# Kernel optimization log

Hardware: AMD Instinct MI355X
Metric: run time of the kernel (lower is better)

Reference implementation:

```python
import jax, jax.numpy as jnp
import numpy as np

B, N, L = 1, 256, 512
D_MSA, D_STATE, D_INNER, D_FF = 256, 64, 32, 1024
H = 4
CA_IDX = 1
SCALE = (D_STATE // H) ** -0.5
BINS = np.array([8.0, 12.0, 16.0, 20.0], dtype=np.float32)
EPS = 1e-5


def _ln(x, g, b):
    m = x.mean(-1, keepdims=True)
    v = ((x - m) ** 2).mean(-1, keepdims=True)
    return (x - m) * jax.lax.rsqrt(v + EPS) * g + b


def setup_inputs() -> dict:
    key = jax.random.key(0)
    ks = jax.random.split(key, 8)
    w = lambda k, shp: (jax.random.normal(k, shp, dtype=jnp.float32) * 0.02)
    return {
        "xyz": jax.random.normal(ks[0], (B, L, 3, 3), dtype=jnp.float32) * 10.0,
        "state": jax.random.normal(ks[1], (B, L, D_STATE), dtype=jnp.float32),
        "msa": jax.random.normal(ks[2], (B, N, L, D_MSA), dtype=jnp.float32),
        "ln_msa_g": jnp.ones((D_MSA,)), "ln_msa_b": jnp.zeros((D_MSA,)),
        "ln_state_g": jnp.ones((D_STATE,)), "ln_state_b": jnp.zeros((D_STATE,)),
        "Wq": w(ks[3], (D_STATE, H * D_INNER)), "bq": jnp.zeros((H * D_INNER,)),
        "Wk": w(ks[4], (D_STATE, H * D_INNER)), "bk": jnp.zeros((H * D_INNER,)),
        "Wv": w(ks[5], (D_MSA, D_MSA)), "bv": jnp.zeros((D_MSA,)),
        "ln_out_g": jnp.ones((D_MSA,)), "ln_out_b": jnp.zeros((D_MSA,)),
        "ff_ln_g": jnp.ones((D_MSA,)), "ff_ln_b": jnp.zeros((D_MSA,)),
        "W1": w(ks[6], (D_MSA, D_FF)), "b1": jnp.zeros((D_FF,)),
        "W2": w(ks[7], (D_FF, D_MSA)), "b2": jnp.zeros((D_MSA,)),
    }


def reference(xyz, state, msa, ln_msa_g, ln_msa_b, ln_state_g, ln_state_b,
              Wq, bq, Wk, bk, Wv, bv, ln_out_g, ln_out_b,
              ff_ln_g, ff_ln_b, W1, b1, W2, b2):
    state_n = _ln(state, ln_state_g, ln_state_b)          # [b,l,ds]
    msa_n = _ln(msa, ln_msa_g, ln_msa_b)                  # [b,n,l,dm]

    q = (state_n @ Wq + bq).reshape(B, L, H, D_INNER).transpose(0, 2, 1, 3)  # bhld
    k = (state_n @ Wk + bk).reshape(B, L, H, D_INNER).transpose(0, 2, 1, 3)
    v = (msa_n @ Wv + bv).reshape(B, N, L, H, D_MSA // H).transpose(0, 3, 1, 2, 4)  # bhnld

    ca = xyz[:, :, CA_IDX]                                # [b,l,3]
    diff = ca[:, :, None, :] - ca[:, None, :, :]
    pdist = jnp.sqrt((diff * diff).sum(-1))               # [b,l,l]
    mask = (pdist[:, None] < jnp.asarray(BINS)[None, :, None, None]).astype(state.dtype)  # [b,h,l,l]

    logits = jnp.einsum('bhid,bhjd->bhij', q * SCALE, k) + (1.0 - mask) * -1e9
    att = jax.nn.softmax(logits, axis=-1)                 # [b,h,i,j]

    out = jnp.einsum('bhij,bhnjd->bhnid', att, v)         # [b,h,n,l,d]
    out = out.transpose(0, 2, 3, 1, 4).reshape(B, N, L, D_MSA)

    msa2 = msa_n + _ln(out, ln_out_g, ln_out_b)
    hdn = jnp.maximum(_ln(msa2, ff_ln_g, ff_ln_b) @ W1 + b1, 0.0)
    return msa2 + hdn @ W2 + b2
```

## Files before the change

kernel.cpp:

```cpp
#include <hip/hip_runtime.h>
#include <stdint.h>

typedef __attribute__((ext_vector_type(8))) short bf16x8;
typedef __attribute__((ext_vector_type(4))) float f32x4;
typedef __attribute__((ext_vector_type(4))) short s16x4;

__device__ __forceinline__ float bf2f(short u) {
  union { float f; unsigned int i; } c; c.i = ((unsigned int)(unsigned short)u) << 16; return c.f;
}
__device__ __forceinline__ short f2bf(float f) {
  union { float f; unsigned int i; } c; c.f = f;
  return (short)((c.i + 0x7FFFu + ((c.i >> 16) & 1u)) >> 16);
}
__device__ __forceinline__ float wredsum(float v) {
#pragma unroll
  for (int o = 32; o; o >>= 1) v += __shfl_xor(v, o);
  return v;
}
__device__ __forceinline__ void gload16(const short* g, short* l) {
  __builtin_amdgcn_global_load_lds(
      (const __attribute__((address_space(1))) unsigned int*)g,
      (__attribute__((address_space(3))) unsigned int*)l, 16, 0, 0);
}

__global__ void k_transpose(const float* __restrict__ in, short* __restrict__ out,
                            int R, int C) {
  int idx = blockIdx.x * 256 + threadIdx.x;
  if (idx >= R * C) return;
  int c = idx / R, r = idx - c * R;
  out[idx] = f2bf(in[(size_t)r * C + c]);
}

__global__ __launch_bounds__(128) void k_qk(
    const float* __restrict__ state, const float* __restrict__ g, const float* __restrict__ b,
    const float* __restrict__ Wq, const float* __restrict__ bq,
    const float* __restrict__ Wk, const float* __restrict__ bk,
    float* __restrict__ qbuf, float* __restrict__ kbuf) {
  __shared__ float sn[64];
  const int l = blockIdx.x, tid = threadIdx.x;
  if (tid < 64) {
    float v = state[l * 64 + tid];
    float mean = wredsum(v) * (1.f / 64.f);
    float d = v - mean;
    float var = wredsum(d * d) * (1.f / 64.f);
    sn[tid] = d * rsqrtf(var + 1e-5f) * g[tid] + b[tid];
  }
  __syncthreads();
  float qa = 0.f, ka = 0.f;
#pragma unroll 8
  for (int k = 0; k < 64; ++k) {
    float s = sn[k];
    qa += s * Wq[k * 128 + tid];
    ka += s * Wk[k * 128 + tid];
  }
  qbuf[l * 128 + tid] = (qa + bq[tid]) * 0.25f;
  kbuf[l * 128 + tid] = ka + bk[tid];
}

__global__ __launch_bounds__(256) void k_att(
    const float* __restrict__ qbuf, const float* __restrict__ kbuf,
    const float* __restrict__ xyz, short* __restrict__ att) {
  __shared__ float qs[32];
  __shared__ float cai[3];
  __shared__ float wm[4], wsm[4];
  const int i = blockIdx.x, h = blockIdx.y, t = threadIdx.x;
  if (t < 32) qs[t] = qbuf[i * 128 + h * 32 + t];
  if (t < 3) cai[t] = xyz[i * 9 + 3 + t];
  __syncthreads();
  const float bin2 = (h == 0) ? 64.f : (h == 1) ? 144.f : (h == 2) ? 256.f : 400.f;
  float lg[2];
#pragma unroll
  for (int p = 0; p < 2; ++p) {
    int j = t + p * 256;
    const float* kr = kbuf + j * 128 + h * 32;
    float a = 0.f;
#pragma unroll 8
    for (int d = 0; d < 32; ++d) a += qs[d] * kr[d];
    float dx = cai[0] - xyz[j * 9 + 3], dy = cai[1] - xyz[j * 9 + 4], dz = cai[2] - xyz[j * 9 + 5];
    float d2 = dx * dx + dy * dy + dz * dz;
    lg[p] = (d2 < bin2) ? a : a - 1e9f;
  }
  const int wave = t >> 6, lane = t & 63;
  float m = fmaxf(lg[0], lg[1]);
#pragma unroll
  for (int o = 32; o; o >>= 1) m = fmaxf(m, __shfl_xor(m, o));
  if (lane == 0) wm[wave] = m;
  __syncthreads();
  m = fmaxf(fmaxf(wm[0], wm[1]), fmaxf(wm[2], wm[3]));
  float e0 = __expf(lg[0] - m), e1 = __expf(lg[1] - m);
  float s = wredsum(e0 + e1);
  if (lane == 0) wsm[wave] = s;
  __syncthreads();
  float inv = 1.f / (wsm[0] + wsm[1] + wsm[2] + wsm[3]);
  size_t base = ((size_t)h * 512 + i) * 512;
  att[base + t] = f2bf(e0 * inv);
  att[base + t + 256] = f2bf(e1 * inv);
}

__global__ __launch_bounds__(256) void k_msaln(
    const float* __restrict__ msa, const float* __restrict__ g, const float* __restrict__ b,
    short* __restrict__ msa_n) {
  const int wave = threadIdx.x >> 6, lane = threadIdx.x & 63;
  const size_t row = (size_t)blockIdx.x * 4 + wave;
  const float4 v = ((const float4*)(msa + row * 256))[lane];
  float mean = wredsum(v.x + v.y + v.z + v.w) * (1.f / 256.f);
  float d0 = v.x - mean, d1 = v.y - mean, d2 = v.z - mean, d3 = v.w - mean;
  float var = wredsum(d0 * d0 + d1 * d1 + d2 * d2 + d3 * d3) * (1.f / 256.f);
  float rs = rsqrtf(var + 1e-5f);
  const int c = lane * 4;
  s16x4 o;
  o[0] = f2bf(d0 * rs * g[c + 0] + b[c + 0]);
  o[1] = f2bf(d1 * rs * g[c + 1] + b[c + 1]);
  o[2] = f2bf(d2 * rs * g[c + 2] + b[c + 2]);
  o[3] = f2bf(d3 * rs * g[c + 3] + b[c + 3]);
  *(s16x4*)(msa_n + row * 256 + c) = o;
}

__global__ __launch_bounds__(256) void k_msa2(
    const short* __restrict__ O, const float* __restrict__ bv,
    const short* __restrict__ msa_n,
    const float* __restrict__ go, const float* __restrict__ bo,
    const float* __restrict__ gf, const float* __restrict__ bfp,
    short* __restrict__ msa2, short* __restrict__ msa2ln) {
  const int wave = threadIdx.x >> 6, lane = threadIdx.x & 63;
  const size_t row = (size_t)blockIdx.x * 4 + wave;
  const int c = lane * 4;
  s16x4 ov = *(const s16x4*)(O + row * 256 + c);
  float t0 = bf2f(ov[0]) + bv[c + 0], t1 = bf2f(ov[1]) + bv[c + 1];
  float t2 = bf2f(ov[2]) + bv[c + 2], t3 = bf2f(ov[3]) + bv[c + 3];
  float mean = wredsum(t0 + t1 + t2 + t3) * (1.f / 256.f);
  float d0 = t0 - mean, d1 = t1 - mean, d2 = t2 - mean, d3 = t3 - mean;
  float var = wredsum(d0 * d0 + d1 * d1 + d2 * d2 + d3 * d3) * (1.f / 256.f);
  float rs = rsqrtf(var + 1e-5f);
  s16x4 nv = *(const s16x4*)(msa_n + row * 256 + c);
  float m0 = bf2f(nv[0]) + d0 * rs * go[c + 0] + bo[c + 0];
  float m1 = bf2f(nv[1]) + d1 * rs * go[c + 1] + bo[c + 1];
  float m2 = bf2f(nv[2]) + d2 * rs * go[c + 2] + bo[c + 2];
  float m3 = bf2f(nv[3]) + d3 * rs * go[c + 3] + bo[c + 3];
  float mean2 = wredsum(m0 + m1 + m2 + m3) * (1.f / 256.f);
  float e0 = m0 - mean2, e1 = m1 - mean2, e2 = m2 - mean2, e3 = m3 - mean2;
  float var2 = wredsum(e0 * e0 + e1 * e1 + e2 * e2 + e3 * e3) * (1.f / 256.f);
  float rs2 = rsqrtf(var2 + 1e-5f);
  s16x4 w1; w1[0] = f2bf(m0); w1[1] = f2bf(m1); w1[2] = f2bf(m2); w1[3] = f2bf(m3);
  *(s16x4*)(msa2 + row * 256 + c) = w1;
  s16x4 w2;
  w2[0] = f2bf(e0 * rs2 * gf[c + 0] + bfp[c + 0]);
  w2[1] = f2bf(e1 * rs2 * gf[c + 1] + bfp[c + 1]);
  w2[2] = f2bf(e2 * rs2 * gf[c + 2] + bfp[c + 2]);
  w2[3] = f2bf(e3 * rs2 * gf[c + 3] + bfp[c + 3]);
  *(s16x4*)(msa2ln + row * 256 + c) = w2;
}

template <int BM, int BN, int WR, int WC, bool ATTN, bool BIAS, bool RELU, bool RES, bool OUTBF>
__global__ __launch_bounds__(256) void gemm_nt(
    const short* __restrict__ A, const short* __restrict__ B, void* __restrict__ Cv,
    const float* __restrict__ bias, const short* __restrict__ res,
    int K, int lda, int ldb, int ldc) {
  constexpr int WM = BM / WR, WN = BN / WC;
  constexpr int MF = WM / 16, NF = WN / 16;
  __shared__ alignas(16) short As[BM * 32];
  __shared__ alignas(16) short Bs[BN * 32];
  const int tid = threadIdx.x;
  const int wave = tid >> 6, lane = tid & 63;
  const int wr = wave / WC, wc = wave % WC;
  size_t offA = 0, offB = 0, offC = 0;
  if (ATTN) {
    const int z = blockIdx.z, h = z & 3, nl = z >> 2;
    offA = (size_t)h * (512 * 512);
    offB = (size_t)(h * 64) * ldb + (size_t)nl * 512;
    offC = (size_t)nl * 512 * ldc + (size_t)h * 64;
  }
  const int rowBase = blockIdx.x * BM;
  const int colBase = blockIdx.y * BN;
  const f32x4 fzero = {0.f, 0.f, 0.f, 0.f};
  f32x4 acc[MF][NF];
#pragma unroll
  for (int m = 0; m < MF; ++m)
#pragma unroll
    for (int n = 0; n < NF; ++n) acc[m][n] = fzero;

  const int srow = lane >> 2;
  const int skoff = (lane & 3) << 3;
  const int fr = lane & 15, fk = (lane >> 4) << 3;

  for (int kt = 0; kt < K; kt += 32) {
    __syncthreads();
    for (int ch = wave; ch < BM / 16; ch += 4) {
      const short* src = A + offA + (size_t)(rowBase + ch * 16 + srow) * lda + kt + skoff;
      gload16(src, &As[ch * 512]);
    }
    for (int ch = wave; ch < BN / 16; ch += 4) {
      const short* src = B + offB + (size_t)(colBase + ch * 16 + srow) * ldb + kt + skoff;
      gload16(src, &Bs[ch * 512]);
    }
    __syncthreads();
    bf16x8 af[MF], bfr[NF];
#pragma unroll
    for (int m = 0; m < MF; ++m)
      af[m] = *(const bf16x8*)&As[(wr * WM + m * 16 + fr) * 32 + fk];
#pragma unroll
    for (int n = 0; n < NF; ++n)
      bfr[n] = *(const bf16x8*)&Bs[(wc * WN + n * 16 + fr) * 32 + fk];
#pragma unroll
    for (int m = 0; m < MF; ++m)
#pragma unroll
      for (int n = 0; n < NF; ++n)
        acc[m][n] = __builtin_amdgcn_mfma_f32_16x16x32_bf16(af[m], bfr[n], acc[m][n], 0, 0, 0);
  }

  const int er = (lane >> 4) << 2;
  const int ec = lane & 15;
#pragma unroll
  for (int m = 0; m < MF; ++m) {
#pragma unroll
    for (int n = 0; n < NF; ++n) {
      const int col = colBase + wc * WN + n * 16 + ec;
      const float bb = BIAS ? bias[col] : 0.f;
#pragma unroll
      for (int j = 0; j < 4; ++j) {
        const int row = rowBase + wr * WM + m * 16 + er + j;
        float v = acc[m][n][j] + bb;
        if (RELU) v = fmaxf(v, 0.f);
        const size_t ci = offC + (size_t)row * ldc + col;
        if (RES) v += bf2f(res[ci]);
        if (OUTBF) ((short*)Cv)[ci] = f2bf(v);
        else ((float*)Cv)[ci] = v;
      }
    }
  }
}

extern "C" void kernel_launch(void* const* d_in, const int* in_sizes, int n_in,
                              void* d_out, int out_size, void* d_ws, size_t ws_size,
                              hipStream_t stream) {
  (void)in_sizes; (void)n_in; (void)out_size;
  const float* xyz  = (const float*)d_in[0];
  const float* state= (const float*)d_in[1];
  const float* msa  = (const float*)d_in[2];
  const float* g_msa= (const float*)d_in[3];
  const float* b_msa= (const float*)d_in[4];
  const float* g_st = (const float*)d_in[5];
  const float* b_st = (const float*)d_in[6];
  const float* Wq   = (const float*)d_in[7];
  const float* bq   = (const float*)d_in[8];
  const float* Wk   = (const float*)d_in[9];
  const float* bk   = (const float*)d_in[10];
  const float* Wv   = (const float*)d_in[11];
  const float* bv   = (const float*)d_in[12];
  const float* g_out= (const float*)d_in[13];
  const float* b_out= (const float*)d_in[14];
  const float* g_ff = (const float*)d_in[15];
  const float* b_ff = (const float*)d_in[16];
  const float* W1   = (const float*)d_in[17];
  const float* b1   = (const float*)d_in[18];
  const float* W2   = (const float*)d_in[19];
  const float* b2   = (const float*)d_in[20];
  float* out = (float*)d_out;

  int NC = 16;
  {
    const size_t per_n = 5ull * 512 * 256 * 2 + 512ull * 1024 * 2;
    const int cands[5] = {1, 2, 4, 8, 16};
    for (int ci = 0; ci < 5; ++ci) {
      size_t need = 8ull * 1024 * 1024 + (size_t)(256 / cands[ci]) * per_n;
      if (need <= ws_size) { NC = cands[ci]; break; }
    }
  }
  const int NB = 256 / NC;

  char* ws = (char*)d_ws;
  size_t off = 0;
  auto alloc = [&](size_t bytes) -> void* {
    void* p = ws + off;
    off = (off + bytes + 255) & ~(size_t)255;
    return p;
  };
  float* qbuf = (float*)alloc(512 * 128 * 4);
  float* kbuf = (float*)alloc(512 * 128 * 4);
  short* att  = (short*)alloc((size_t)4 * 512 * 512 * 2);
  short* Wvt  = (short*)alloc(65536 * 2);
  short* W1t  = (short*)alloc(262144 * 2);
  short* W2t  = (short*)alloc(262144 * 2);
  const size_t chrows = (size_t)NB * 512;
  short* msa_n_c = (short*)alloc(chrows * 256 * 2);
  short* Vt_c    = (short*)alloc(chrows * 256 * 2);
  short* O_c     = (short*)alloc(chrows * 256 * 2);
  short* msa2_c  = (short*)alloc(chrows * 256 * 2);
  short* msa2ln_c= (short*)alloc(chrows * 256 * 2);
  short* hdn_c   = (short*)alloc(chrows * 1024 * 2);

  k_transpose<<<(65536 + 255) / 256, 256, 0, stream>>>(Wv, Wvt, 256, 256);
  k_transpose<<<(262144 + 255) / 256, 256, 0, stream>>>(W1, W1t, 256, 1024);
  k_transpose<<<(262144 + 255) / 256, 256, 0, stream>>>(W2, W2t, 1024, 256);
  k_qk<<<512, 128, 0, stream>>>(state, g_st, b_st, Wq, bq, Wk, bk, qbuf, kbuf);
  k_att<<<dim3(512, 4), 256, 0, stream>>>(qbuf, kbuf, xyz, att);

  for (int cc = 0; cc < NC; ++cc) {
    const size_t nOff = (size_t)cc * NB;
    k_msaln<<<NB * 128, 256, 0, stream>>>(msa + nOff * 512 * 256, g_msa, b_msa, msa_n_c);
    gemm_nt<128, 128, 2, 2, false, false, false, false, true>
        <<<dim3(2, NB * 4), 256, 0, stream>>>(Wvt, msa_n_c, Vt_c, nullptr, nullptr,
                                              256, 256, 256, NB * 512);
    gemm_nt<128, 64, 2, 2, true, false, false, false, true>
        <<<dim3(4, 1, NB * 4), 256, 0, stream>>>(att, Vt_c, O_c, nullptr, nullptr,
                                                 512, 512, NB * 512, 256);
    k_msa2<<<NB * 128, 256, 0, stream>>>(O_c, bv, msa_n_c, g_out, b_out, g_ff, b_ff,
                                         msa2_c, msa2ln_c);
    gemm_nt<128, 128, 2, 2, false, true, true, false, true>
        <<<dim3(NB * 4, 8), 256, 0, stream>>>(msa2ln_c, W1t, hdn_c, b1, nullptr,
                                              256, 256, 256, 1024);
    gemm_nt<128, 128, 2, 2, false, true, false, true, false>
        <<<dim3(NB * 4, 2), 256, 0, stream>>>(hdn_c, W2t, out + nOff * 512 * 256, b2, msa2_c,
                                              1024, 1024, 1024, 256);
  }
}
```

Before: 778.7 us.

## Fuse FFN GEMMs into one kernel, double-buffer swizzled GEMM, tile transposes

Replaces the two FFN GEMMs with a fused kernel that keeps each 64-row hidden slice in LDS, so the 1024-wide hidden activation is never written to or read back from global memory. The generic GEMM moves to a K=64 step with double-buffered, XOR-swizzled LDS staging, which overlaps global loads with MFMA and reduces bank conflicts. The V projection now writes a per-sequence transposed layout, and the weight transposes use a shared-memory tiled kernel. The fused FFN uses a large LDS footprint and 512 threads per block, which may limit occupancy.

```diff
diff --git a/kernel.cpp b/kernel.cpp
--- a/kernel.cpp
+++ b/kernel.cpp
@@ -23,12 +23,18 @@
       (__attribute__((address_space(3))) unsigned int*)l, 16, 0, 0);
 }
 
-__global__ void k_transpose(const float* __restrict__ in, short* __restrict__ out,
-                            int R, int C) {
-  int idx = blockIdx.x * 256 + threadIdx.x;
-  if (idx >= R * C) return;
-  int c = idx / R, r = idx - c * R;
-  out[idx] = f2bf(in[(size_t)r * C + c]);
+__global__ __launch_bounds__(256) void k_transpose(const float* __restrict__ in,
+                                                   short* __restrict__ out, int R, int C) {
+  __shared__ float t[32][33];
+  const int bx = blockIdx.x, by = blockIdx.y;
+  const int tx = threadIdx.x & 31, ty = threadIdx.x >> 5;
+#pragma unroll
+  for (int i = 0; i < 4; ++i)
+    t[ty + i * 8][tx] = in[(size_t)(by * 32 + ty + i * 8) * C + bx * 32 + tx];
+  __syncthreads();
+#pragma unroll
+  for (int i = 0; i < 4; ++i)
+    out[(size_t)(bx * 32 + ty + i * 8) * R + by * 32 + tx] = f2bf(t[tx][ty + i * 8]);
 }
 
 __global__ __launch_bounds__(128) void k_qk(
@@ -151,27 +157,38 @@
   *(s16x4*)(msa2ln + row * 256 + c) = w2;
 }
 
-template <int BM, int BN, int WR, int WC, bool ATTN, bool BIAS, bool RELU, bool RES, bool OUTBF>
+template <int BM, int BN, int MODE>
 __global__ __launch_bounds__(256) void gemm_nt(
-    const short* __restrict__ A, const short* __restrict__ B, void* __restrict__ Cv,
-    const float* __restrict__ bias, const short* __restrict__ res,
+    const short* __restrict__ A, const short* __restrict__ B, short* __restrict__ C,
     int K, int lda, int ldb, int ldc) {
-  constexpr int WM = BM / WR, WN = BN / WC;
+  constexpr int WM = BM / 2, WN = BN / 2;
   constexpr int MF = WM / 16, NF = WN / 16;
-  __shared__ alignas(16) short As[BM * 32];
-  __shared__ alignas(16) short Bs[BN * 32];
-  const int tid = threadIdx.x;
-  const int wave = tid >> 6, lane = tid & 63;
-  const int wr = wave / WC, wc = wave % WC;
+  __shared__ alignas(16) short As[2][BM * 64];
+  __shared__ alignas(16) short Bs[2][BN * 64];
+  const int tid = threadIdx.x, wave = tid >> 6, lane = tid & 63;
+  const int wr = wave >> 1, wc = wave & 1;
+  const int fr = lane & 15;
   size_t offA = 0, offB = 0, offC = 0;
-  if (ATTN) {
+  if (MODE == 1) {
     const int z = blockIdx.z, h = z & 3, nl = z >> 2;
     offA = (size_t)h * (512 * 512);
-    offB = (size_t)(h * 64) * ldb + (size_t)nl * 512;
-    offC = (size_t)nl * 512 * ldc + (size_t)h * 64;
-  }
-  const int rowBase = blockIdx.x * BM;
-  const int colBase = blockIdx.y * BN;
+    offB = (size_t)nl * (256 * 512) + (size_t)(h * 64) * 512;
+    offC = (size_t)nl * (512 * 256) + (size_t)(h * 64);
+  } else if (MODE == 2) {
+    const size_t z = blockIdx.z;
+    offB = z * (512 * 256);
+    offC = z * (256 * 512);
+  }
+  const int rowBase = blockIdx.x * BM, colBase = blockIdx.y * BN;
+
+  auto stage = [&](const short* G, size_t goff, int ld, int rb, int kt, short* dst, int nrow) {
+    for (int ch = wave; ch < nrow / 8; ch += 4) {
+      const int r = ch * 8 + (lane >> 3);
+      const int kel = (((lane & 7) * 16) ^ ((r & 7) << 4)) >> 1;
+      gload16(G + goff + (size_t)(rb + r) * ld + kt + kel, dst + ch * 512);
+    }
+  };
+
   const f32x4 fzero = {0.f, 0.f, 0.f, 0.f};
   f32x4 acc[MF][NF];
 #pragma unroll
@@ -179,55 +196,221 @@
 #pragma unroll
     for (int n = 0; n < NF; ++n) acc[m][n] = fzero;
 
-  const int srow = lane >> 2;
-  const int skoff = (lane & 3) << 3;
-  const int fr = lane & 15, fk = (lane >> 4) << 3;
-
-  for (int kt = 0; kt < K; kt += 32) {
+  stage(A, offA, lda, rowBase, 0, As[0], BM);
+  stage(B, offB, ldb, colBase, 0, Bs[0], BN);
+  int buf = 0;
+  for (int kt = 0; kt < K; kt += 64) {
     __syncthreads();
-    for (int ch = wave; ch < BM / 16; ch += 4) {
-      const short* src = A + offA + (size_t)(rowBase + ch * 16 + srow) * lda + kt + skoff;
-      gload16(src, &As[ch * 512]);
-    }
-    for (int ch = wave; ch < BN / 16; ch += 4) {
-      const short* src = B + offB + (size_t)(colBase + ch * 16 + srow) * ldb + kt + skoff;
-      gload16(src, &Bs[ch * 512]);
-    }
-    __syncthreads();
-    bf16x8 af[MF], bfr[NF];
+    if (kt + 64 < K) {
+      stage(A, offA, lda, rowBase, kt + 64, As[buf ^ 1], BM);
+      stage(B, offB, ldb, colBase, kt + 64, Bs[buf ^ 1], BN);
+    }
+    bf16x8 af[MF][2], bfr[NF][2];
 #pragma unroll
     for (int m = 0; m < MF; ++m)
-      af[m] = *(const bf16x8*)&As[(wr * WM + m * 16 + fr) * 32 + fk];
+#pragma unroll
+      for (int kk = 0; kk < 2; ++kk) {
+        const int r = wr * WM + m * 16 + fr;
+        const int b = kk * 64 + (lane >> 4) * 16;
+        af[m][kk] = *(const bf16x8*)&As[buf][r * 64 + ((b ^ ((r & 7) << 4)) >> 1)];
+      }
 #pragma unroll
     for (int n = 0; n < NF; ++n)
-      bfr[n] = *(const bf16x8*)&Bs[(wc * WN + n * 16 + fr) * 32 + fk];
+#pragma unroll
+      for (int kk = 0; kk < 2; ++kk) {
+        const int r = wc * WN + n * 16 + fr;
+        const int b = kk * 64 + (lane >> 4) * 16;
+        bfr[n][kk] = *(const bf16x8*)&Bs[buf][r * 64 + ((b ^ ((r & 7) << 4)) >> 1)];
+      }
 #pragma unroll
     for (int m = 0; m < MF; ++m)
 #pragma unroll
       for (int n = 0; n < NF; ++n)
-        acc[m][n] = __builtin_amdgcn_mfma_f32_16x16x32_bf16(af[m], bfr[n], acc[m][n], 0, 0, 0);
-  }
-
-  const int er = (lane >> 4) << 2;
-  const int ec = lane & 15;
-#pragma unroll
-  for (int m = 0; m < MF; ++m) {
+#pragma unroll
+        for (int kk = 0; kk < 2; ++kk)
+          acc[m][n] = __builtin_amdgcn_mfma_f32_16x16x32_bf16(af[m][kk], bfr[n][kk], acc[m][n], 0, 0, 0);
+    buf ^= 1;
+  }
+
+  const int er = (lane >> 4) << 2, ec = lane & 15;
+#pragma unroll
+  for (int m = 0; m < MF; ++m)
 #pragma unroll
     for (int n = 0; n < NF; ++n) {
       const int col = colBase + wc * WN + n * 16 + ec;
-      const float bb = BIAS ? bias[col] : 0.f;
 #pragma unroll
       for (int j = 0; j < 4; ++j) {
         const int row = rowBase + wr * WM + m * 16 + er + j;
-        float v = acc[m][n][j] + bb;
-        if (RELU) v = fmaxf(v, 0.f);
-        const size_t ci = offC + (size_t)row * ldc + col;
-        if (RES) v += bf2f(res[ci]);
-        if (OUTBF) ((short*)Cv)[ci] = f2bf(v);
-        else ((float*)Cv)[ci] = v;
-      }
-    }
-  }
+        C[offC + (size_t)row * ldc + col] = f2bf(acc[m][n][j]);
+      }
+    }
+}
+
+__global__ __launch_bounds__(512) void k_ffn(
+    const short* __restrict__ msa2ln, const short* __restrict__ msa2,
+    const short* __restrict__ W1t, const short* __restrict__ W2t,
+    const float* __restrict__ b1, const float* __restrict__ b2,
+    float* __restrict__ out) {
+  __shared__ alignas(16) short ring[2][16384];
+  __shared__ alignas(16) short P[8192];
+  const int tid = threadIdx.x, wave = tid >> 6, lane = tid & 63;
+  const int wr = wave >> 2, wc = wave & 3;
+  const int fr = lane & 15, er = (lane >> 4) << 2, ec = fr;
+  const size_t rowBase = (size_t)blockIdx.x * 64;
+
+  for (int ch = wave; ch < 32; ch += 8) {
+    const int r = ch * 2 + (lane >> 5);
+    const int kel = (((lane & 31) * 16) ^ ((r & 7) << 4)) >> 1;
+    gload16(msa2ln + (rowBase + r) * 256 + kel, &ring[0][ch * 512]);
+  }
+  __syncthreads();
+  bf16x8 areg[2][8];
+#pragma unroll
+  for (int m = 0; m < 2; ++m)
+#pragma unroll
+    for (int kk = 0; kk < 8; ++kk) {
+      const int r = wr * 32 + m * 16 + fr;
+      const int b = kk * 64 + (lane >> 4) * 16;
+      areg[m][kk] = *(const bf16x8*)&ring[0][r * 256 + ((b ^ ((r & 7) << 4)) >> 1)];
+    }
+  __syncthreads();
+
+  auto stageW = [&](int s, short* dst) {
+    const int f8s = s >> 2, q = s & 3;
+    if (q < 2) {
+      for (int ch = wave; ch < 32; ch += 8) {
+        const int r = ch * 4 + (lane >> 4);
+        const int kel = (((lane & 15) * 16) ^ ((r & 7) << 4)) >> 1;
+        gload16(W1t + (size_t)(f8s * 128 + r) * 256 + q * 128 + kel, dst + ch * 512);
+      }
+    } else {
+      for (int ch = wave; ch < 32; ch += 8) {
+        const int r = ch * 8 + (lane >> 3);
+        const int kel = (((lane & 7) * 16) ^ ((r & 7) << 4)) >> 1;
+        gload16(W2t + (size_t)r * 1024 + f8s * 128 + (q - 2) * 64 + kel, dst + ch * 512);
+      }
+    }
+  };
+
+  const f32x4 fzero = {0.f, 0.f, 0.f, 0.f};
+  f32x4 acc2[2][4];
+#pragma unroll
+  for (int m = 0; m < 2; ++m)
+#pragma unroll
+    for (int n = 0; n < 4; ++n) acc2[m][n] = fzero;
+
+#define G1STEP(QC)                                                                   \
+  {                                                                                  \
+    bf16x8 bfr[2][4];                                                                \
+    _Pragma("unroll") for (int n = 0; n < 2; ++n) {                                  \
+      _Pragma("unroll") for (int kk = 0; kk < 4; ++kk) {                             \
+        const int r = wc * 32 + n * 16 + fr;                                         \
+        const int b = kk * 64 + (lane >> 4) * 16;                                    \
+        bfr[n][kk] = *(const bf16x8*)&buf[r * 128 + ((b ^ ((r & 7) << 4)) >> 1)];    \
+      }                                                                              \
+    }                                                                                \
+    _Pragma("unroll") for (int m = 0; m < 2; ++m) {                                  \
+      _Pragma("unroll") for (int n = 0; n < 2; ++n) {                                \
+        _Pragma("unroll") for (int kk = 0; kk < 4; ++kk)                             \
+          acc1[m][n] = __builtin_amdgcn_mfma_f32_16x16x32_bf16(                      \
+              areg[m][QC * 4 + kk], bfr[n][kk], acc1[m][n], 0, 0, 0);                \
+      }                                                                              \
+    }                                                                                \
+  }
+
+#define G2STEP(CC)                                                                   \
+  {                                                                                  \
+    bf16x8 a2[2][2], bfr[4][2];                                                      \
+    _Pragma("unroll") for (int m = 0; m < 2; ++m) {                                  \
+      _Pragma("unroll") for (int kk = 0; kk < 2; ++kk) {                             \
+        const int r = wr * 32 + m * 16 + fr;                                         \
+        const int b = CC * 128 + kk * 64 + (lane >> 4) * 16;                         \
+        a2[m][kk] = *(const bf16x8*)&P[r * 128 + ((b ^ ((r & 7) << 4)) >> 1)];       \
+      }                                                                              \
+    }                                                                                \
+    _Pragma("unroll") for (int n = 0; n < 4; ++n) {                                  \
+      _Pragma("unroll") for (int kk = 0; kk < 2; ++kk) {                             \
+        const int r = wc * 64 + n * 16 + fr;                                         \
+        const int b = kk * 64 + (lane >> 4) * 16;                                    \
+        bfr[n][kk] = *(const bf16x8*)&buf[r * 64 + ((b ^ ((r & 7) << 4)) >> 1)];     \
+      }                                                                              \
+    }                                                                                \
+    _Pragma("unroll") for (int m = 0; m < 2; ++m) {                                  \
+      _Pragma("unroll") for (int n = 0; n < 4; ++n) {                                \
+        _Pragma("unroll") for (int kk = 0; kk < 2; ++kk)                             \
+          acc2[m][n] = __builtin_amdgcn_mfma_f32_16x16x32_bf16(                      \
+              a2[m][kk], bfr[n][kk], acc2[m][n], 0, 0, 0);                           \
+      }                                                                              \
+    }                                                                                \
+  }
+
+  int s = 0;
+  stageW(0, ring[0]);
+#pragma unroll 1
+  for (int f8 = 0; f8 < 8; ++f8) {
+    f32x4 acc1[2][2];
+#pragma unroll
+    for (int m = 0; m < 2; ++m)
+#pragma unroll
+      for (int n = 0; n < 2; ++n) acc1[m][n] = fzero;
+    float b1v[2];
+    {
+      __syncthreads();
+      stageW(s + 1, ring[(s + 1) & 1]);
+      b1v[0] = b1[f8 * 128 + wc * 32 + ec];
+      b1v[1] = b1[f8 * 128 + wc * 32 + 16 + ec];
+      const short* buf = ring[s & 1];
+      G1STEP(0);
+      ++s;
+    }
+    {
+      __syncthreads();
+      stageW(s + 1, ring[(s + 1) & 1]);
+      const short* buf = ring[s & 1];
+      G1STEP(1);
+      ++s;
+    }
+#pragma unroll
+    for (int m = 0; m < 2; ++m)
+#pragma unroll
+      for (int n = 0; n < 2; ++n) {
+        const int col2 = (wc * 32 + n * 16 + ec) * 2;
+#pragma unroll
+        for (int j = 0; j < 4; ++j) {
+          const int row = wr * 32 + m * 16 + er + j;
+          P[row * 128 + ((col2 ^ ((row & 7) << 4)) >> 1)] = f2bf(fmaxf(acc1[m][n][j] + b1v[n], 0.f));
+        }
+      }
+    {
+      __syncthreads();
+      stageW(s + 1, ring[(s + 1) & 1]);
+      const short* buf = ring[s & 1];
+      G2STEP(0);
+      ++s;
+    }
+    {
+      __syncthreads();
+      if (s + 1 < 32) stageW(s + 1, ring[(s + 1) & 1]);
+      const short* buf = ring[s & 1];
+      G2STEP(1);
+      ++s;
+    }
+  }
+#undef G1STEP
+#undef G2STEP
+
+#pragma unroll
+  for (int m = 0; m < 2; ++m)
+#pragma unroll
+    for (int n = 0; n < 4; ++n) {
+      const int col = wc * 64 + n * 16 + ec;
+      const float bb = b2[col];
+#pragma unroll
+      for (int j = 0; j < 4; ++j) {
+        const size_t row = rowBase + wr * 32 + m * 16 + er + j;
+        out[row * 256 + col] = acc2[m][n][j] + bb + bf2f(msa2[row * 256 + col]);
+      }
+    }
 }
 
 extern "C" void kernel_launch(void* const* d_in, const int* in_sizes, int n_in,
@@ -259,7 +442,7 @@
 
   int NC = 16;
   {
-    const size_t per_n = 5ull * 512 * 256 * 2 + 512ull * 1024 * 2;
+    const size_t per_n = 5ull * 512 * 256 * 2;
     const int cands[5] = {1, 2, 4, 8, 16};
     for (int ci = 0; ci < 5; ++ci) {
       size_t need = 8ull * 1024 * 1024 + (size_t)(256 / cands[ci]) * per_n;
@@ -287,30 +470,23 @@
   short* O_c     = (short*)alloc(chrows * 256 * 2);
   short* msa2_c  = (short*)alloc(chrows * 256 * 2);
   short* msa2ln_c= (short*)alloc(chrows * 256 * 2);
-  short* hdn_c   = (short*)alloc(chrows * 1024 * 2);
-
-  k_transpose<<<(65536 + 255) / 256, 256, 0, stream>>>(Wv, Wvt, 256, 256);
-  k_transpose<<<(262144 + 255) / 256, 256, 0, stream>>>(W1, W1t, 256, 1024);
-  k_transpose<<<(262144 + 255) / 256, 256, 0, stream>>>(W2, W2t, 1024, 256);
+
+  k_transpose<<<dim3(8, 8), 256, 0, stream>>>(Wv, Wvt, 256, 256);
+  k_transpose<<<dim3(32, 8), 256, 0, stream>>>(W1, W1t, 256, 1024);
+  k_transpose<<<dim3(8, 32), 256, 0, stream>>>(W2, W2t, 1024, 256);
   k_qk<<<512, 128, 0, stream>>>(state, g_st, b_st, Wq, bq, Wk, bk, qbuf, kbuf);
   k_att<<<dim3(512, 4), 256, 0, stream>>>(qbuf, kbuf, xyz, att);
 
   for (int cc = 0; cc < NC; ++cc) {
     const size_t nOff = (size_t)cc * NB;
     k_msaln<<<NB * 128, 256, 0, stream>>>(msa + nOff * 512 * 256, g_msa, b_msa, msa_n_c);
-    gemm_nt<128, 128, 2, 2, false, false, false, false, true>
-        <<<dim3(2, NB * 4), 256, 0, stream>>>(Wvt, msa_n_c, Vt_c, nullptr, nullptr,
-                                              256, 256, 256, NB * 512);
-    gemm_nt<128, 64, 2, 2, true, false, false, false, true>
-        <<<dim3(4, 1, NB * 4), 256, 0, stream>>>(att, Vt_c, O_c, nullptr, nullptr,
-                                                 512, 512, NB * 512, 256);
+    gemm_nt<128, 128, 2><<<dim3(2, 4, NB), 256, 0, stream>>>(
+        Wvt, msa_n_c, Vt_c, 256, 256, 256, 512);
+    gemm_nt<128, 64, 1><<<dim3(4, 1, NB * 4), 256, 0, stream>>>(
+        att, Vt_c, O_c, 512, 512, 512, 256);
     k_msa2<<<NB * 128, 256, 0, stream>>>(O_c, bv, msa_n_c, g_out, b_out, g_ff, b_ff,
                                          msa2_c, msa2ln_c);
-    gemm_nt<128, 128, 2, 2, false, true, true, false, true>
-        <<<dim3(NB * 4, 8), 256, 0, stream>>>(msa2ln_c, W1t, hdn_c, b1, nullptr,
-                                              256, 256, 256, 1024);
-    gemm_nt<128, 128, 2, 2, false, true, false, true, false>
-        <<<dim3(NB * 4, 2), 256, 0, stream>>>(hdn_c, W2t, out + nOff * 512 * 256, b2, msa2_c,
-                                              1024, 1024, 1024, 256);
-  }
-}
+    k_ffn<<<NB * 8, 512, 0, stream>>>(msa2ln_c, msa2_c, W1t, W2t, b1, b2,
+                                      out + nOff * 512 * 256);
+  }
+}
```

After: 718.3 us. 7.8% less time.
